# Performance work log

Hardware: AMD Instinct MI355X
Metric: run time of the kernel (lower is better)

The kernel has to match this reference:

```python
import jax, jax.numpy as jnp
import numpy as np

EMBED = 1024
HEADS = 16
HEAD_SIZE = EMBED // HEADS
B, T = 2, 2048
EPS = 1e-5


def layer_norm(x, g, b):
    mu = jnp.mean(x, axis=-1, keepdims=True)
    var = jnp.var(x, axis=-1, keepdims=True)
    return (x - mu) * jax.lax.rsqrt(var + EPS) * g + b


def setup_inputs() -> dict:
    key = jax.random.key(0)
    ks = jax.random.split(key, 12)
    s = 0.02
    return {
        "x": jax.random.normal(ks[0], (B, T, EMBED), jnp.float32),
        "Wq": s * jax.random.normal(ks[1], (EMBED, EMBED), jnp.float32),
        "Wk": s * jax.random.normal(ks[2], (EMBED, EMBED), jnp.float32),
        "Wv": s * jax.random.normal(ks[3], (EMBED, EMBED), jnp.float32),
        "Wo": s * jax.random.normal(ks[4], (EMBED, EMBED), jnp.float32),
        "bo": jnp.zeros((EMBED,), jnp.float32),
        "W1": s * jax.random.normal(ks[5], (EMBED, 4 * EMBED), jnp.float32),
        "b1": jnp.zeros((4 * EMBED,), jnp.float32),
        "W2": s * jax.random.normal(ks[6], (4 * EMBED, EMBED), jnp.float32),
        "b2": jnp.zeros((EMBED,), jnp.float32),
        "ln1_g": jnp.ones((EMBED,), jnp.float32),
        "ln1_b": jnp.zeros((EMBED,), jnp.float32),
        "ln2_g": jnp.ones((EMBED,), jnp.float32),
        "ln2_b": jnp.zeros((EMBED,), jnp.float32),
    }


def reference(x, Wq, Wk, Wv, Wo, bo, W1, b1, W2, b2, ln1_g, ln1_b, ln2_g, ln2_b):
    # --- multi-head causal self-attention on ln1(x) ---
    h = layer_norm(x, ln1_g, ln1_b)                      # [B,T,D]
    q = (h @ Wq).reshape(B, T, HEADS, HEAD_SIZE)         # per-head Q (concat layout)
    k = (h @ Wk).reshape(B, T, HEADS, HEAD_SIZE)
    v = (h @ Wv).reshape(B, T, HEADS, HEAD_SIZE)
    scores = jnp.einsum("bqhd,bkhd->bhqk", q, k) / jnp.sqrt(
        jnp.asarray(HEAD_SIZE, x.dtype)
    )                                                    # [B,H,T,T]
    causal = jnp.tril(jnp.ones((T, T), bool))
    scores = jnp.where(causal, scores, -jnp.inf)
    wei = jax.nn.softmax(scores, axis=-1)
    attn = jnp.einsum("bhqk,bkhd->bqhd", wei, v).reshape(B, T, EMBED)
    x = x + attn @ Wo + bo                               # residual (dropout=0)
    # --- feed-forward on ln2(x) ---
    h2 = layer_norm(x, ln2_g, ln2_b)
    ff = jax.nn.relu(h2 @ W1 + b1) @ W2 + b2
    return x + ff
```

## Files before the change

kernel.cpp:

```cpp
#include <hip/hip_runtime.h>


typedef __bf16 bf16;
typedef __attribute__((ext_vector_type(8))) __bf16 bf16x8;
typedef __attribute__((ext_vector_type(4))) __bf16 bf16x4;
typedef __attribute__((ext_vector_type(4))) short  shortx4;
typedef __attribute__((ext_vector_type(4))) float  floatx4;

__device__ __forceinline__ short f2bf_bits(float x) {
  return __builtin_bit_cast(short, (bf16)x);
}

__device__ __forceinline__ void gl2lds16(const bf16* g, bf16* l) {
  __builtin_amdgcn_global_load_lds((const __attribute__((address_space(1))) void*)g,
                                   (__attribute__((address_space(3))) void*)l, 16, 0, 0);
}

__device__ __forceinline__ void barx() {
  asm volatile("" ::: "memory");
  __builtin_amdgcn_s_barrier();
  asm volatile("" ::: "memory");
}

__global__ __launch_bounds__(256) void prep_kernel(
    const float* __restrict__ Wq, const float* __restrict__ Wk,
    const float* __restrict__ Wv, const float* __restrict__ Wo,
    const float* __restrict__ W1, const float* __restrict__ W2,
    bf16* __restrict__ WqkvT, bf16* __restrict__ WoT,
    bf16* __restrict__ W1T, bf16* __restrict__ W2T,
    const float* __restrict__ x, const float* __restrict__ ln1g,
    const float* __restrict__ ln1b, bf16* __restrict__ h1)
{
  int id = blockIdx.x;
  if (id >= 12288) {
    const int row = id - 12288, t = threadIdx.x;
    const float* xr = x + (size_t)row * 1024;
    float4 v = *(const float4*)(xr + t * 4);
    float s  = v.x + v.y + v.z + v.w;
    float s2 = v.x * v.x + v.y * v.y + v.z * v.z + v.w * v.w;
    #pragma unroll
    for (int off = 1; off < 64; off <<= 1) {
      s  += __shfl_xor(s, off);
      s2 += __shfl_xor(s2, off);
    }
    __shared__ float ps[4], ps2[4];
    int wv = t >> 6;
    if ((t & 63) == 0) { ps[wv] = s; ps2[wv] = s2; }
    __syncthreads();
    s  = ps[0] + ps[1] + ps[2] + ps[3];
    s2 = ps2[0] + ps2[1] + ps2[2] + ps2[3];
    const float mu = s * (1.0f / 1024.0f);
    const float rstd = rsqrtf(s2 * (1.0f / 1024.0f) - mu * mu + 1e-5f);
    float4 gv = *(const float4*)(ln1g + t * 4);
    float4 bv = *(const float4*)(ln1b + t * 4);
    bf16x4 o;
    o[0] = (bf16)((v.x - mu) * rstd * gv.x + bv.x);
    o[1] = (bf16)((v.y - mu) * rstd * gv.y + bv.y);
    o[2] = (bf16)((v.z - mu) * rstd * gv.z + bv.z);
    o[3] = (bf16)((v.w - mu) * rstd * gv.w + bv.w);
    *(bf16x4*)(h1 + (size_t)row * 1024 + t * 4) = o;
    return;
  }
  const float* src; bf16* dst; int K, N, tile;
  if (id < 4096) {
    K = 1024; N = 1024; tile = id & 1023;
    int wsel = id >> 10;
    src = (wsel == 0) ? Wq : (wsel == 1) ? Wk : (wsel == 2) ? Wv : Wo;
    dst = (wsel < 3) ? (WqkvT + (size_t)wsel * 1024 * 1024) : WoT;
  } else if (id < 8192) {
    K = 1024; N = 4096; tile = id - 4096; src = W1; dst = W1T;
  } else {
    K = 4096; N = 1024; tile = id - 8192; src = W2; dst = W2T;
  }
  int ntn = N >> 5;
  int k0 = (tile / ntn) * 32, n0 = (tile % ntn) * 32;
  __shared__ float tl[32][33];
  int tr = threadIdx.x >> 3, tc = (threadIdx.x & 7) * 4;
  float4 v = *(const float4*)(src + (size_t)(k0 + tr) * N + n0 + tc);
  tl[tr][tc + 0] = v.x; tl[tr][tc + 1] = v.y; tl[tr][tc + 2] = v.z; tl[tr][tc + 3] = v.w;
  __syncthreads();
  bf16x4 o = { (bf16)tl[tc + 0][tr], (bf16)tl[tc + 1][tr],
               (bf16)tl[tc + 2][tr], (bf16)tl[tc + 3][tr] };
  *(bf16x4*)(dst + (size_t)(n0 + tr) * K + k0 + tc) = o;
}

__device__ __forceinline__ void gemm_core(
    const bf16* __restrict__ A, const bf16* __restrict__ Bt,
    int Ktot, int k0, int k1, bf16* As, bf16* Bs, floatx4 (&acc)[4][4])
{
  const int tid = threadIdx.x, lane = tid & 63, wv = tid >> 6;
  const int li = lane & 15, g = lane >> 4;
  const int wm = wv >> 1, wn = wv & 1;
  const int srow = wv * 16 + (lane >> 2);
  const int scol = (lane & 3) * 8;
  const bf16* aP = A  + (size_t)srow * Ktot + scol;
  const bf16* bP = Bt + (size_t)srow * Ktot + scol;
  bf16* AsW = As + wv * 512;
  bf16* BsW = Bs + wv * 512;
  for (int kt = k0; kt < k1; kt += 64) {
    gl2lds16(aP + kt,                          AsW);
    gl2lds16(aP + kt + (size_t)64 * Ktot,      AsW + 2048);
    gl2lds16(aP + kt + 32,                     AsW + 4096);
    gl2lds16(aP + kt + 32 + (size_t)64 * Ktot, AsW + 6144);
    gl2lds16(bP + kt,                          BsW);
    gl2lds16(bP + kt + (size_t)64 * Ktot,      BsW + 2048);
    gl2lds16(bP + kt + 32,                     BsW + 4096);
    gl2lds16(bP + kt + 32 + (size_t)64 * Ktot, BsW + 6144);
    __syncthreads();
    #pragma unroll
    for (int hh = 0; hh < 2; ++hh) {
      const bf16* Ap = As + hh * 4096;
      const bf16* Bp = Bs + hh * 4096;
      bf16x8 af[4], bfr[4];
      #pragma unroll
      for (int r = 0; r < 4; ++r)
        af[r] = *(const bf16x8*)(Ap + (wm * 64 + r * 16 + li) * 32 + g * 8);
      #pragma unroll
      for (int c = 0; c < 4; ++c)
        bfr[c] = *(const bf16x8*)(Bp + (wn * 64 + c * 16 + li) * 32 + g * 8);
      #pragma unroll
      for (int r = 0; r < 4; ++r)
        #pragma unroll
        for (int c = 0; c < 4; ++c)
          acc[r][c] = __builtin_amdgcn_mfma_f32_16x16x32_bf16(bfr[c], af[r], acc[r][c], 0, 0, 0);
    }
    __syncthreads();
  }
}

__global__ __launch_bounds__(256) void gemm_splitk(
    const bf16* __restrict__ A, const bf16* __restrict__ Bt,
    bf16* __restrict__ Cp, int M, int N, int Ktot, int Kc)
{
  __shared__ bf16 As[8192];
  __shared__ bf16 Bs[8192];
  const int lane = threadIdx.x & 63, wv = threadIdx.x >> 6;
  const int li = lane & 15, g = lane >> 4;
  const int m0 = blockIdx.x * 128, n0 = blockIdx.y * 128;
  const int z = blockIdx.z;
  const int wm = wv >> 1, wn = wv & 1;
  floatx4 acc[4][4] = {};
  gemm_core(A + (size_t)m0 * Ktot, Bt + (size_t)n0 * Ktot, Ktot,
            z * Kc, (z + 1) * Kc, As, Bs, acc);
  bf16* C = Cp + (size_t)z * M * N;
  #pragma unroll
  for (int r = 0; r < 4; ++r) {
    int rowC = m0 + wm * 64 + r * 16 + li;
    #pragma unroll
    for (int c = 0; c < 4; ++c) {
      int colC = n0 + wn * 64 + c * 16 + g * 4;
      bf16x4 ov = { (bf16)acc[r][c][0], (bf16)acc[r][c][1],
                    (bf16)acc[r][c][2], (bf16)acc[r][c][3] };
      *(bf16x4*)(C + (size_t)rowC * N + colC) = ov;
    }
  }
}


#define MFMA_PHASE(RH, CH, BB)                                                  \
  do {                                                                          \
    __builtin_amdgcn_s_setprio(1);                                              \
    _Pragma("unroll") for (int ks = 0; ks < 2; ++ks)                            \
      _Pragma("unroll") for (int r = 0; r < 4; ++r)                             \
        _Pragma("unroll") for (int c = 0; c < 2; ++c)                           \
          acc[(RH) * 4 + r][(CH) * 2 + c] =                                     \
            __builtin_amdgcn_mfma_f32_16x16x32_bf16(                            \
                BB[c][ks], af[r][ks], acc[(RH) * 4 + r][(CH) * 2 + c], 0, 0, 0);\
    __builtin_amdgcn_s_setprio(0);                                              \
  } while (0)

__device__ __forceinline__ void gemm8_core(
    const bf16* __restrict__ A, const bf16* __restrict__ Bt,
    int K, int k0, int k1, bf16* lds, floatx4 (&acc)[8][4])
{
  const int lane = threadIdx.x & 63, wv = threadIdx.x >> 6;
  const int li = lane & 15, g = lane >> 4;
  const int wm2 = wv >> 2, wn4 = wv & 3;
  const int nt = (k1 - k0) >> 6;

  const int srow  = wv * 16 + (lane >> 3);
  const int schnk = ((lane & 7) ^ (lane >> 3)) * 8;
  const bf16* aSrc = A  + (size_t)srow * K + k0 + schnk;
  const bf16* bSrc = Bt + (size_t)srow * K + k0 + schnk;
  const size_t row8 = (size_t)8 * K;
  bf16* ldsB = lds + 32768;

  const int xk0 = ((0 + g) ^ (li & 7)) * 8;
  const int xk1 = ((4 + g) ^ (li & 7)) * 8;

  auto stA = [&](int t, int h) {
    if (t < nt) {
      const bf16* gp = aSrc + (size_t)(h * 128) * K + (t << 6);
      bf16* lp = lds + (((t & 1) * 2 + h) << 13) + wv * 1024;
      gl2lds16(gp, lp);
      gl2lds16(gp + row8, lp + 512);
    }
  };
  auto stB = [&](int t, int h) {
    if (t < nt) {
      const bf16* gp = bSrc + (size_t)(h * 128) * K + (t << 6);
      bf16* lp = ldsB + (((t & 1) * 2 + h) << 13) + wv * 1024;
      gl2lds16(gp, lp);
      gl2lds16(gp + row8, lp + 512);
    }
  };

  bf16x8 af[4][2], bA[2][2], bB[2][2];
  auto ldA = [&](int b, int RH) {
    const bf16* base = lds + ((b * 2 + RH) << 13) + (wm2 * 64 + li) * 64;
    #pragma unroll
    for (int r = 0; r < 4; ++r) {
      af[r][0] = *(const bf16x8*)(base + r * 1024 + xk0);
      af[r][1] = *(const bf16x8*)(base + r * 1024 + xk1);
    }
  };
  auto ldB = [&](int b, int CH, bf16x8 (&bb)[2][2]) {
    const bf16* base = ldsB + ((b * 2 + CH) << 13) + (wn4 * 32 + li) * 64;
    #pragma unroll
    for (int c = 0; c < 2; ++c) {
      bb[c][0] = *(const bf16x8*)(base + c * 1024 + xk0);
      bb[c][1] = *(const bf16x8*)(base + c * 1024 + xk1);
    }
  };

  stA(0, 0); stB(0, 0); stB(0, 1); stA(0, 1);
  stA(1, 0); stB(1, 0);
  asm volatile("s_waitcnt vmcnt(4)" ::: "memory");
  barx();

  for (int t = 0; t < nt; ++t) {
    const int b = t & 1;
    ldA(b, 0); ldB(b, 0, bA);
    stB(t + 1, 1);
    barx();
    MFMA_PHASE(0, 0, bA);
    barx();
    ldB(b, 1, bB);
    stA(t + 1, 1);
    asm volatile("s_waitcnt vmcnt(8)" ::: "memory");
    barx();
    MFMA_PHASE(0, 1, bB);
    barx();
    ldA(b, 1);
    stA(t + 2, 0);
    barx();
    MFMA_PHASE(1, 0, bA);
    barx();
    stB(t + 2, 0);
    asm volatile("s_waitcnt vmcnt(6)" ::: "memory");
    barx();
    MFMA_PHASE(1, 1, bB);
    barx();
  }
}

__global__ __launch_bounds__(512, 2) void gemm8_ffn1(
    const bf16* __restrict__ A, const bf16* __restrict__ Bt,
    const float* __restrict__ bias, bf16* __restrict__ C,
    int M, int N, int K)
{
  __shared__ bf16 lds8[65536];
  const int m0 = blockIdx.x * 256, n0 = blockIdx.y * 256;
  floatx4 acc[8][4] = {};
  gemm8_core(A + (size_t)m0 * K, Bt + (size_t)n0 * K, K, 0, K, lds8, acc);
  const int lane = threadIdx.x & 63, wv = threadIdx.x >> 6;
  const int li = lane & 15, g = lane >> 4;
  const int wm2 = wv >> 2, wn4 = wv & 3;
  #pragma unroll
  for (int ar = 0; ar < 8; ++ar) {
    int rowC = m0 + (ar >> 2) * 128 + wm2 * 64 + (ar & 3) * 16 + li;
    #pragma unroll
    for (int ac = 0; ac < 4; ++ac) {
      int colC = n0 + (ac >> 1) * 128 + wn4 * 32 + (ac & 1) * 16 + g * 4;
      float4 bv = *(const float4*)(bias + colC);
      bf16x4 ov = { (bf16)fmaxf(acc[ar][ac][0] + bv.x, 0.f),
                    (bf16)fmaxf(acc[ar][ac][1] + bv.y, 0.f),
                    (bf16)fmaxf(acc[ar][ac][2] + bv.z, 0.f),
                    (bf16)fmaxf(acc[ar][ac][3] + bv.w, 0.f) };
      *(bf16x4*)(C + (size_t)rowC * N + colC) = ov;
    }
  }
}

__global__ __launch_bounds__(512, 2) void gemm8_qkv(
    const bf16* __restrict__ A, const bf16* __restrict__ Bt,
    bf16* __restrict__ qkv, bf16* __restrict__ VtG)
{
  const int K = 1024;
  __shared__ bf16 lds8[65536];
  const int m0 = blockIdx.x * 256, n0 = blockIdx.y * 256;
  floatx4 acc[8][4] = {};
  gemm8_core(A + (size_t)m0 * K, Bt + (size_t)n0 * K, K, 0, K, lds8, acc);
  const int lane = threadIdx.x & 63, wv = threadIdx.x >> 6;
  const int li = lane & 15, g = lane >> 4;
  const int wm2 = wv >> 2, wn4 = wv & 3;
  if (n0 < 2048) {
    #pragma unroll
    for (int ar = 0; ar < 8; ++ar) {
      int rowC = m0 + (ar >> 2) * 128 + wm2 * 64 + (ar & 3) * 16 + li;
      #pragma unroll
      for (int ac = 0; ac < 4; ++ac) {
        int colC = n0 + (ac >> 1) * 128 + wn4 * 32 + (ac & 1) * 16 + g * 4;
        bf16x4 ov = { (bf16)acc[ar][ac][0], (bf16)acc[ar][ac][1],
                      (bf16)acc[ar][ac][2], (bf16)acc[ar][ac][3] };
        *(bf16x4*)(qkv + (size_t)rowC * 3072 + colC) = ov;
      }
    }
  } else {
    #pragma unroll
    for (int ar = 0; ar < 8; ++ar) {
      int rowC = m0 + (ar >> 2) * 128 + wm2 * 64 + (ar & 3) * 16 + li;
      int key = rowC & 2047, bq = rowC >> 11;
      #pragma unroll
      for (int ac = 0; ac < 4; ++ac) {
        int vcol0 = n0 + (ac >> 1) * 128 + wn4 * 32 + (ac & 1) * 16 + g * 4 - 2048;
        #pragma unroll
        for (int e = 0; e < 4; ++e) {
          int vcol = vcol0 + e;
          int hh = vcol >> 6, d = vcol & 63;
          VtG[((size_t)(bq * 16 + hh) * 64 + d) * 2048 + key] = (bf16)acc[ar][ac][e];
        }
      }
    }
  }
}

__global__ __launch_bounds__(512, 2) void gemm8_splitk(
    const bf16* __restrict__ A, const bf16* __restrict__ Bt,
    bf16* __restrict__ Cp, int M, int N, int Ktot, int Kc)
{
  __shared__ bf16 lds8[65536];
  const int m0 = blockIdx.x * 256, n0 = blockIdx.y * 256;
  const int z = blockIdx.z;
  floatx4 acc[8][4] = {};
  gemm8_core(A + (size_t)m0 * Ktot, Bt + (size_t)n0 * Ktot, Ktot,
             z * Kc, (z + 1) * Kc, lds8, acc);
  const int lane = threadIdx.x & 63, wv = threadIdx.x >> 6;
  const int li = lane & 15, g = lane >> 4;
  const int wm2 = wv >> 2, wn4 = wv & 3;
  bf16* C = Cp + (size_t)z * M * N;
  #pragma unroll
  for (int ar = 0; ar < 8; ++ar) {
    int rowC = m0 + (ar >> 2) * 128 + wm2 * 64 + (ar & 3) * 16 + li;
    #pragma unroll
    for (int ac = 0; ac < 4; ++ac) {
      int colC = n0 + (ac >> 1) * 128 + wn4 * 32 + (ac & 1) * 16 + g * 4;
      bf16x4 ov = { (bf16)acc[ar][ac][0], (bf16)acc[ar][ac][1],
                    (bf16)acc[ar][ac][2], (bf16)acc[ar][ac][3] };
      *(bf16x4*)(C + (size_t)rowC * N + colC) = ov;
    }
  }
}

__global__ __launch_bounds__(256) void combine_wo_ln2(
    const bf16* __restrict__ P, const float* __restrict__ bo,
    const float* __restrict__ x, const float* __restrict__ gam,
    const float* __restrict__ bet, float* __restrict__ x2, bf16* __restrict__ h2)
{
  const int row = blockIdx.x, t = threadIdx.x;
  const size_t base = (size_t)row * 1024 + t * 4;
  float4 v = *(const float4*)(x + base);
  bf16x4 p0 = *(const bf16x4*)(P + base);
  bf16x4 p1 = *(const bf16x4*)(P + 4194304 + base);
  float4 bv = *(const float4*)(bo + t * 4);
  v.x += (float)p0[0] + (float)p1[0] + bv.x;
  v.y += (float)p0[1] + (float)p1[1] + bv.y;
  v.z += (float)p0[2] + (float)p1[2] + bv.z;
  v.w += (float)p0[3] + (float)p1[3] + bv.w;
  *(float4*)(x2 + base) = v;
  float s  = v.x + v.y + v.z + v.w;
  float s2 = v.x * v.x + v.y * v.y + v.z * v.z + v.w * v.w;
  #pragma unroll
  for (int off = 1; off < 64; off <<= 1) {
    s  += __shfl_xor(s, off);
    s2 += __shfl_xor(s2, off);
  }
  __shared__ float ps[4], ps2[4];
  int wv = t >> 6;
  if ((t & 63) == 0) { ps[wv] = s; ps2[wv] = s2; }
  __syncthreads();
  s  = ps[0] + ps[1] + ps[2] + ps[3];
  s2 = ps2[0] + ps2[1] + ps2[2] + ps2[3];
  const float mu = s * (1.0f / 1024.0f);
  const float rstd = rsqrtf(s2 * (1.0f / 1024.0f) - mu * mu + 1e-5f);
  float4 gv = *(const float4*)(gam + t * 4);
  float4 bb = *(const float4*)(bet + t * 4);
  bf16x4 o;
  o[0] = (bf16)((v.x - mu) * rstd * gv.x + bb.x);
  o[1] = (bf16)((v.y - mu) * rstd * gv.y + bb.y);
  o[2] = (bf16)((v.z - mu) * rstd * gv.z + bb.z);
  o[3] = (bf16)((v.w - mu) * rstd * gv.w + bb.w);
  *(bf16x4*)(h2 + base) = o;
}

__global__ __launch_bounds__(256) void combine_ffn2(
    const bf16* __restrict__ P, const float* __restrict__ b2,
    const float* __restrict__ x2, float* __restrict__ out)
{
  const size_t i = ((size_t)blockIdx.x * 256 + threadIdx.x) * 4;
  const int col = (int)(i & 1023);
  float4 acc = *(const float4*)(x2 + i);
  float4 bv = *(const float4*)(b2 + col);
  acc.x += bv.x; acc.y += bv.y; acc.z += bv.z; acc.w += bv.w;
  #pragma unroll
  for (int z = 0; z < 4; ++z) {
    bf16x4 p = *(const bf16x4*)(P + (size_t)z * 4194304 + i);
    acc.x += (float)p[0]; acc.y += (float)p[1];
    acc.z += (float)p[2]; acc.w += (float)p[3];
  }
  *(float4*)(out + i) = acc;
}

__global__ __launch_bounds__(256, 2) void attn_kernel(
    const bf16* __restrict__ qkv, const bf16* __restrict__ VtG,
    bf16* __restrict__ attnb)
{
  __shared__ bf16 Ks[2][64 * 72];
  __shared__ bf16 Vt[2][64 * 72];
  const int t = threadIdx.x, lane = t & 63, wv = t >> 6;
  const int li = lane & 15, g = lane >> 4;
  const int p = blockIdx.x & 15, h = (blockIdx.x >> 4) & 15, b = blockIdx.x >> 8;
  const int row0 = b << 11;
  const int tlo = p * 4 + wv, thi = 127 - tlo;
  const int q0l = tlo << 4, q0h = thi << 4;
  const size_t qkvbase = (size_t)row0 * 3072 + (size_t)h * 64;
  const bf16* vgbase = VtG + (size_t)(b * 16 + h) * 64 * 2048;

  const bf16* qpl = qkv + qkvbase + (size_t)(q0l + li) * 3072 + g * 8;
  const bf16* qph = qkv + qkvbase + (size_t)(q0h + li) * 3072 + g * 8;
  bf16x8 bl0 = *(const bf16x8*)(qpl), bl1 = *(const bf16x8*)(qpl + 32);
  bf16x8 bh0 = *(const bf16x8*)(qph), bh1 = *(const bf16x8*)(qph + 32);

  floatx4 ol[4] = {}, oh[4] = {};
  float ll = 0.f, lh = 0.f;
  const int cmax = 31 - p;

  const int krow0 = t >> 3, kdc = (t & 7) * 8;
  const int vd = t >> 2, vkg = (t & 3) * 16;
  bf16x8 kv0, kv1, vv0, vv1;

  auto ld = [&](int c) {
    const size_t kb = qkvbase + (size_t)(c * 64) * 3072 + 1024;
    kv0 = *(const bf16x8*)(qkv + kb + (size_t)krow0 * 3072 + kdc);
    kv1 = *(const bf16x8*)(qkv + kb + (size_t)(krow0 + 32) * 3072 + kdc);
    const bf16* vg = vgbase + (size_t)vd * 2048 + c * 64 + vkg;
    vv0 = *(const bf16x8*)(vg);
    vv1 = *(const bf16x8*)(vg + 8);
  };
  auto wr = [&](int buf) {
    *(bf16x8*)(Ks[buf] + krow0 * 72 + kdc)        = kv0;
    *(bf16x8*)(Ks[buf] + (krow0 + 32) * 72 + kdc) = kv1;
    *(bf16x8*)(Vt[buf] + vd * 72 + vkg)           = vv0;
    *(bf16x8*)(Vt[buf] + vd * 72 + vkg + 8)       = vv1;
  };

  auto proc = [&](const bf16* KsB, const bf16* VtB,
                  const bf16x8& bq0, const bf16x8& bq1, float& l_i,
                  floatx4 (&o)[4], int qg, int k0, bool diag) {
    floatx4 sv[4];
    #pragma unroll
    for (int s = 0; s < 4; ++s) {
      const bf16* kr = KsB + (s * 16 + li) * 72 + g * 8;
      bf16x8 a0 = *(const bf16x8*)(kr);
      bf16x8 a1 = *(const bf16x8*)(kr + 32);
      floatx4 z = {0.f, 0.f, 0.f, 0.f};
      z = __builtin_amdgcn_mfma_f32_16x16x32_bf16(a0, bq0, z, 0, 0, 0);
      z = __builtin_amdgcn_mfma_f32_16x16x32_bf16(a1, bq1, z, 0, 0, 0);
      sv[s] = z;
    }
    float pv[4][4];
    float rs = 0.f;
    #pragma unroll
    for (int s = 0; s < 4; ++s)
      #pragma unroll
      for (int e = 0; e < 4; ++e) {
        float val = __expf(sv[s][e] * 0.125f - 4.0f);
        if (diag) {
          int kg = k0 + s * 16 + g * 4 + e;
          val = (kg <= qg) ? val : 0.0f;
        }
        pv[s][e] = val;
        rs += val;
      }
    rs += __shfl_xor(rs, 16);
    rs += __shfl_xor(rs, 32);
    l_i += rs;
    #pragma unroll
    for (int s = 0; s < 4; ++s) {
      shortx4 bp = { f2bf_bits(pv[s][0]), f2bf_bits(pv[s][1]),
                     f2bf_bits(pv[s][2]), f2bf_bits(pv[s][3]) };
      #pragma unroll
      for (int c = 0; c < 4; ++c) {
        shortx4 av = *(const shortx4*)(VtB + (c * 16 + li) * 72 + s * 16 + g * 4);
        o[c] = __builtin_amdgcn_mfma_f32_16x16x16bf16_1k(av, bp, o[c], 0, 0, 0);
      }
    }
  };

  ld(0);
  wr(0);
  __syncthreads();
  int buf = 0;
  for (int c = 0; c <= cmax; ++c) {
    if (c < cmax) ld(c + 1);
    proc(Ks[buf], Vt[buf], bh0, bh1, lh, oh, q0h + li, c * 64, c == cmax);
    if (c <= p) proc(Ks[buf], Vt[buf], bl0, bl1, ll, ol, q0l + li, c * 64, c == p);
    if (c < cmax) wr(buf ^ 1);
    __syncthreads();
    buf ^= 1;
  }

  const float invh = 1.0f / lh, invl = 1.0f / ll;
  #pragma unroll
  for (int c = 0; c < 4; ++c) {
    bf16x4 ovh = { (bf16)(oh[c][0] * invh), (bf16)(oh[c][1] * invh),
                   (bf16)(oh[c][2] * invh), (bf16)(oh[c][3] * invh) };
    *(bf16x4*)(attnb + (size_t)(row0 + q0h + li) * 1024 + h * 64 + c * 16 + g * 4) = ovh;
    bf16x4 ovl = { (bf16)(ol[c][0] * invl), (bf16)(ol[c][1] * invl),
                   (bf16)(ol[c][2] * invl), (bf16)(ol[c][3] * invl) };
    *(bf16x4*)(attnb + (size_t)(row0 + q0l + li) * 1024 + h * 64 + c * 16 + g * 4) = ovl;
  }
}

extern "C" void kernel_launch(void* const* d_in, const int* in_sizes, int n_in,
                              void* d_out, int out_size, void* d_ws, size_t ws_size,
                              hipStream_t stream) {
  (void)in_sizes; (void)n_in; (void)out_size; (void)ws_size;
  const float* x    = (const float*)d_in[0];
  const float* Wq   = (const float*)d_in[1];
  const float* Wk   = (const float*)d_in[2];
  const float* Wv   = (const float*)d_in[3];
  const float* Wo   = (const float*)d_in[4];
  const float* bo   = (const float*)d_in[5];
  const float* W1   = (const float*)d_in[6];
  const float* b1   = (const float*)d_in[7];
  const float* W2   = (const float*)d_in[8];
  const float* b2   = (const float*)d_in[9];
  const float* ln1g = (const float*)d_in[10];
  const float* ln1b = (const float*)d_in[11];
  const float* ln2g = (const float*)d_in[12];
  const float* ln2b = (const float*)d_in[13];
  float* out = (float*)d_out;
  char* ws = (char*)d_ws;

  constexpr size_t OFF_WQKVT = 0;
  constexpr size_t OFF_WOT   = OFF_WQKVT + 3072ull * 1024 * 2;
  constexpr size_t OFF_W1T   = OFF_WOT   + 1024ull * 1024 * 2;
  constexpr size_t OFF_W2T   = OFF_W1T   + 4096ull * 1024 * 2;
  constexpr size_t OFF_H1    = OFF_W2T   + 1024ull * 4096 * 2;
  constexpr size_t OFF_QKV   = OFF_H1    + 4096ull * 1024 * 2;
  constexpr size_t OFF_ATT   = OFF_QKV   + 4096ull * 3072 * 2;
  constexpr size_t OFF_X2    = OFF_ATT   + 4096ull * 1024 * 2;
  constexpr size_t OFF_H2    = OFF_X2    + 4096ull * 1024 * 4;
  constexpr size_t OFF_F1    = OFF_H2    + 4096ull * 1024 * 2;
  constexpr size_t OFF_PART  = OFF_F1    + 4096ull * 4096 * 2;
  constexpr size_t OFF_VTG   = OFF_PART  + 4ull * 4096 * 1024 * 2;

  bf16*  WqkvT = (bf16*)(ws + OFF_WQKVT);
  bf16*  WoT   = (bf16*)(ws + OFF_WOT);
  bf16*  W1T   = (bf16*)(ws + OFF_W1T);
  bf16*  W2T   = (bf16*)(ws + OFF_W2T);
  bf16*  h1    = (bf16*)(ws + OFF_H1);
  bf16*  qkv   = (bf16*)(ws + OFF_QKV);
  bf16*  attnb = (bf16*)(ws + OFF_ATT);
  float* x2    = (float*)(ws + OFF_X2);
  bf16*  h2    = (bf16*)(ws + OFF_H2);
  bf16*  f1    = (bf16*)(ws + OFF_F1);
  bf16*  part  = (bf16*)(ws + OFF_PART);
  bf16*  vtg   = (bf16*)(ws + OFF_VTG);

  prep_kernel<<<16384, 256, 0, stream>>>(Wq, Wk, Wv, Wo, W1, W2,
                                         WqkvT, WoT, W1T, W2T, x, ln1g, ln1b, h1);
  gemm8_qkv<<<dim3(16, 12), 512, 0, stream>>>(h1, WqkvT, qkv, vtg);
  attn_kernel<<<512, 256, 0, stream>>>(qkv, vtg, attnb);
  gemm_splitk<<<dim3(32, 8, 2), 256, 0, stream>>>(attnb, WoT, part, 4096, 1024, 1024, 512);
  combine_wo_ln2<<<4096, 256, 0, stream>>>(part, bo, x, ln2g, ln2b, x2, h2);
  gemm8_ffn1<<<dim3(16, 16), 512, 0, stream>>>(h2, W1T, b1, f1, 4096, 4096, 1024);
  gemm8_splitk<<<dim3(16, 4, 4), 512, 0, stream>>>(f1, W2T, part, 4096, 1024, 4096, 1024);
  combine_ffn2<<<4096, 256, 0, stream>>>(part, b2, x2, out);
}
```

Before: 324.7 us.

## Split causal attention across key-range blocks with partial-sum combine kernel

Replaces the paired high/low query-tile causal balancing with one query tile per block. Late query tiles (p>=16) have their key range split into two halves written as fp32 partial outputs and row sums, and a new combine kernel merges them. Grid grows from 512 to 1536 blocks with an occupancy hint of 4, LDS row padding shrinks from 72 to 68, and setprio is wrapped around the MFMA sections. The aim is more parallelism and better latency hiding, at the cost of an extra launch, fp32 partial traffic through workspace reused from the F1 buffer, and possible LDS bank conflicts from the new stride.

```diff
diff --git a/kernel.cpp b/kernel.cpp
--- a/kernel.cpp
+++ b/kernel.cpp
@@ -156,7 +156,6 @@
   }
 }
 
-
 #define MFMA_PHASE(RH, CH, BB)                                                  \
   do {                                                                          \
     __builtin_amdgcn_s_setprio(1);                                              \
@@ -411,29 +410,36 @@
   *(float4*)(out + i) = acc;
 }
 
-__global__ __launch_bounds__(256, 2) void attn_kernel(
+__global__ __launch_bounds__(256, 4) void attn_kernel(
     const bf16* __restrict__ qkv, const bf16* __restrict__ VtG,
-    bf16* __restrict__ attnb)
-{
-  __shared__ bf16 Ks[2][64 * 72];
-  __shared__ bf16 Vt[2][64 * 72];
+    bf16* __restrict__ attnb, float* __restrict__ oPart, float* __restrict__ lPart)
+{
+  __shared__ bf16 Ks[2][64 * 68];
+  __shared__ bf16 Vt[2][64 * 68];
   const int t = threadIdx.x, lane = t & 63, wv = t >> 6;
   const int li = lane & 15, g = lane >> 4;
-  const int p = blockIdx.x & 15, h = (blockIdx.x >> 4) & 15, b = blockIdx.x >> 8;
+
+  const int xl = blockIdx.x & 7;
+  const int r_ = blockIdx.x >> 3;
+  const int g2 = r_ & 3, w = r_ >> 2;
+  const int bh = g2 * 8 + xl;
+  const int b = bh >> 4, h = bh & 15;
+  int p, sl;
+  if (w < 16)      { p = 31 - w; sl = 0; }
+  else if (w < 32) { p = 47 - w; sl = 1; }
+  else             { p = 47 - w; sl = 0; }
+
+  const int tq = p * 4 + wv;
+  const int q0 = tq << 4;
   const int row0 = b << 11;
-  const int tlo = p * 4 + wv, thi = 127 - tlo;
-  const int q0l = tlo << 4, q0h = thi << 4;
   const size_t qkvbase = (size_t)row0 * 3072 + (size_t)h * 64;
   const bf16* vgbase = VtG + (size_t)(b * 16 + h) * 64 * 2048;
 
-  const bf16* qpl = qkv + qkvbase + (size_t)(q0l + li) * 3072 + g * 8;
-  const bf16* qph = qkv + qkvbase + (size_t)(q0h + li) * 3072 + g * 8;
-  bf16x8 bl0 = *(const bf16x8*)(qpl), bl1 = *(const bf16x8*)(qpl + 32);
-  bf16x8 bh0 = *(const bf16x8*)(qph), bh1 = *(const bf16x8*)(qph + 32);
-
-  floatx4 ol[4] = {}, oh[4] = {};
-  float ll = 0.f, lh = 0.f;
-  const int cmax = 31 - p;
+  const bf16* qp = qkv + qkvbase + (size_t)(q0 + li) * 3072 + g * 8;
+  bf16x8 bq0 = *(const bf16x8*)(qp), bq1 = *(const bf16x8*)(qp + 32);
+
+  floatx4 o[4] = {};
+  float l = 0.f;
 
   const int krow0 = t >> 3, kdc = (t & 7) * 8;
   const int vd = t >> 2, vkg = (t & 3) * 16;
@@ -447,79 +453,106 @@
     vv0 = *(const bf16x8*)(vg);
     vv1 = *(const bf16x8*)(vg + 8);
   };
-  auto wr = [&](int buf) {
-    *(bf16x8*)(Ks[buf] + krow0 * 72 + kdc)        = kv0;
-    *(bf16x8*)(Ks[buf] + (krow0 + 32) * 72 + kdc) = kv1;
-    *(bf16x8*)(Vt[buf] + vd * 72 + vkg)           = vv0;
-    *(bf16x8*)(Vt[buf] + vd * 72 + vkg + 8)       = vv1;
+  auto wr = [&](int bufi) {
+    *(bf16x8*)(Ks[bufi] + krow0 * 68 + kdc)        = kv0;
+    *(bf16x8*)(Ks[bufi] + (krow0 + 32) * 68 + kdc) = kv1;
+    *(bf16x8*)(Vt[bufi] + vd * 68 + vkg)           = vv0;
+    *(bf16x8*)(Vt[bufi] + vd * 68 + vkg + 8)       = vv1;
   };
 
-  auto proc = [&](const bf16* KsB, const bf16* VtB,
-                  const bf16x8& bq0, const bf16x8& bq1, float& l_i,
-                  floatx4 (&o)[4], int qg, int k0, bool diag) {
+  auto proc = [&](const bf16* KsB, const bf16* VtB, int k0, bool diag) {
     floatx4 sv[4];
-    #pragma unroll
-    for (int s = 0; s < 4; ++s) {
-      const bf16* kr = KsB + (s * 16 + li) * 72 + g * 8;
+    __builtin_amdgcn_s_setprio(1);
+    #pragma unroll
+    for (int s4 = 0; s4 < 4; ++s4) {
+      const bf16* kr = KsB + (s4 * 16 + li) * 68 + g * 8;
       bf16x8 a0 = *(const bf16x8*)(kr);
       bf16x8 a1 = *(const bf16x8*)(kr + 32);
       floatx4 z = {0.f, 0.f, 0.f, 0.f};
       z = __builtin_amdgcn_mfma_f32_16x16x32_bf16(a0, bq0, z, 0, 0, 0);
       z = __builtin_amdgcn_mfma_f32_16x16x32_bf16(a1, bq1, z, 0, 0, 0);
-      sv[s] = z;
-    }
+      sv[s4] = z;
+    }
+    __builtin_amdgcn_s_setprio(0);
     float pv[4][4];
     float rs = 0.f;
-    #pragma unroll
-    for (int s = 0; s < 4; ++s)
+    const int qg = q0 + li;
+    #pragma unroll
+    for (int s4 = 0; s4 < 4; ++s4)
       #pragma unroll
       for (int e = 0; e < 4; ++e) {
-        float val = __expf(sv[s][e] * 0.125f - 4.0f);
+        float val = __expf(sv[s4][e] * 0.125f - 4.0f);
         if (diag) {
-          int kg = k0 + s * 16 + g * 4 + e;
+          int kg = k0 + s4 * 16 + g * 4 + e;
           val = (kg <= qg) ? val : 0.0f;
         }
-        pv[s][e] = val;
+        pv[s4][e] = val;
         rs += val;
       }
     rs += __shfl_xor(rs, 16);
     rs += __shfl_xor(rs, 32);
-    l_i += rs;
-    #pragma unroll
-    for (int s = 0; s < 4; ++s) {
-      shortx4 bp = { f2bf_bits(pv[s][0]), f2bf_bits(pv[s][1]),
-                     f2bf_bits(pv[s][2]), f2bf_bits(pv[s][3]) };
+    l += rs;
+    __builtin_amdgcn_s_setprio(1);
+    #pragma unroll
+    for (int s4 = 0; s4 < 4; ++s4) {
+      shortx4 bp = { f2bf_bits(pv[s4][0]), f2bf_bits(pv[s4][1]),
+                     f2bf_bits(pv[s4][2]), f2bf_bits(pv[s4][3]) };
       #pragma unroll
       for (int c = 0; c < 4; ++c) {
-        shortx4 av = *(const shortx4*)(VtB + (c * 16 + li) * 72 + s * 16 + g * 4);
+        shortx4 av = *(const shortx4*)(VtB + (c * 16 + li) * 68 + s4 * 16 + g * 4);
         o[c] = __builtin_amdgcn_mfma_f32_16x16x16bf16_1k(av, bp, o[c], 0, 0, 0);
       }
     }
+    __builtin_amdgcn_s_setprio(0);
   };
 
-  ld(0);
-  wr(0);
+  const int c0 = sl ? 16 : 0;
+  const int cend = (sl == 0 && p >= 16) ? 16 : (p + 1);
+  ld(c0); wr(0);
   __syncthreads();
   int buf = 0;
-  for (int c = 0; c <= cmax; ++c) {
-    if (c < cmax) ld(c + 1);
-    proc(Ks[buf], Vt[buf], bh0, bh1, lh, oh, q0h + li, c * 64, c == cmax);
-    if (c <= p) proc(Ks[buf], Vt[buf], bl0, bl1, ll, ol, q0l + li, c * 64, c == p);
-    if (c < cmax) wr(buf ^ 1);
+  for (int c = c0; c < cend; ++c) {
+    if (c + 1 < cend) ld(c + 1);
+    proc(Ks[buf], Vt[buf], c * 64, c == p);
+    if (c + 1 < cend) wr(buf ^ 1);
     __syncthreads();
     buf ^= 1;
   }
 
-  const float invh = 1.0f / lh, invl = 1.0f / ll;
-  #pragma unroll
-  for (int c = 0; c < 4; ++c) {
-    bf16x4 ovh = { (bf16)(oh[c][0] * invh), (bf16)(oh[c][1] * invh),
-                   (bf16)(oh[c][2] * invh), (bf16)(oh[c][3] * invh) };
-    *(bf16x4*)(attnb + (size_t)(row0 + q0h + li) * 1024 + h * 64 + c * 16 + g * 4) = ovh;
-    bf16x4 ovl = { (bf16)(ol[c][0] * invl), (bf16)(ol[c][1] * invl),
-                   (bf16)(ol[c][2] * invl), (bf16)(ol[c][3] * invl) };
-    *(bf16x4*)(attnb + (size_t)(row0 + q0l + li) * 1024 + h * 64 + c * 16 + g * 4) = ovl;
-  }
+  if (p < 16) {
+    const float inv = 1.0f / l;
+    #pragma unroll
+    for (int c = 0; c < 4; ++c) {
+      bf16x4 ov = { (bf16)(o[c][0] * inv), (bf16)(o[c][1] * inv),
+                    (bf16)(o[c][2] * inv), (bf16)(o[c][3] * inv) };
+      *(bf16x4*)(attnb + (size_t)(row0 + q0 + li) * 1024 + h * 64 + c * 16 + g * 4) = ov;
+    }
+  } else {
+    const int prow = b * 1024 + (q0 + li - 1024);
+    float* oP = oPart + ((size_t)sl * 2048 + prow) * 1024 + h * 64;
+    #pragma unroll
+    for (int c = 0; c < 4; ++c)
+      *(floatx4*)(oP + c * 16 + g * 4) = o[c];
+    if (g == 0)
+      lPart[((size_t)sl * 2048 + prow) * 16 + h] = l;
+  }
+}
+
+__global__ __launch_bounds__(256) void combine_attn(
+    const float* __restrict__ oPart, const float* __restrict__ lPart,
+    bf16* __restrict__ attnb)
+{
+  const int prow = blockIdx.x, t = threadIdx.x;
+  const int col = t * 4, h = t >> 4;
+  const size_t base = (size_t)prow * 1024 + col;
+  float4 o0 = *(const float4*)(oPart + base);
+  float4 o1 = *(const float4*)(oPart + (size_t)2048 * 1024 + base);
+  float l = lPart[prow * 16 + h] + lPart[2048 * 16 + prow * 16 + h];
+  const float inv = 1.0f / l;
+  const int b = prow >> 10, rr = 1024 + (prow & 1023);
+  bf16x4 ov = { (bf16)((o0.x + o1.x) * inv), (bf16)((o0.y + o1.y) * inv),
+                (bf16)((o0.z + o1.z) * inv), (bf16)((o0.w + o1.w) * inv) };
+  *(bf16x4*)(attnb + ((size_t)(b * 2048 + rr)) * 1024 + col) = ov;
 }
 
 extern "C" void kernel_launch(void* const* d_in, const int* in_sizes, int n_in,
@@ -568,11 +601,14 @@
   bf16*  f1    = (bf16*)(ws + OFF_F1);
   bf16*  part  = (bf16*)(ws + OFF_PART);
   bf16*  vtg   = (bf16*)(ws + OFF_VTG);
+  float* oPart = (float*)(ws + OFF_F1);
+  float* lPart = (float*)(ws + OFF_F1 + 2ull * 2048 * 1024 * 4);
 
   prep_kernel<<<16384, 256, 0, stream>>>(Wq, Wk, Wv, Wo, W1, W2,
                                          WqkvT, WoT, W1T, W2T, x, ln1g, ln1b, h1);
   gemm8_qkv<<<dim3(16, 12), 512, 0, stream>>>(h1, WqkvT, qkv, vtg);
-  attn_kernel<<<512, 256, 0, stream>>>(qkv, vtg, attnb);
+  attn_kernel<<<1536, 256, 0, stream>>>(qkv, vtg, attnb, oPart, lPart);
+  combine_attn<<<2048, 256, 0, stream>>>(oPart, lPart, attnb);
   gemm_splitk<<<dim3(32, 8, 2), 256, 0, stream>>>(attnb, WoT, part, 4096, 1024, 1024, 512);
   combine_wo_ln2<<<4096, 256, 0, stream>>>(part, bo, x, ln2g, ln2b, x2, h2);
   gemm8_ffn1<<<dim3(16, 16), 512, 0, stream>>>(h2, W1T, b1, f1, 4096, 4096, 1024);
```

New measurement: 365.9 us. 12.7% more time.
